# Kernel optimization log

Measured on AMD Instinct MI355X. Metric: run time of the kernel, lower is better.

The kernel has to match this reference:

```python
import jax, jax.numpy as jnp
import numpy as np

N, T, F = 64, 2048, 256
PAD_VALUE = 0.0  # mode='constant'


def setup_inputs() -> dict:
    key = jax.random.key(0)
    kx, ks, kl = jax.random.split(key, 3)
    x = jax.random.normal(kx, (N, T, F), dtype=jnp.float32)
    slices = jnp.sort(jax.random.randint(ks, (N, 2), 0, T, dtype=jnp.int64), axis=-1)
    lens = jax.random.randint(kl, (N,), 0, T, dtype=jnp.int64)
    return {"x": x, "slices": slices, "lens": lens}


def reference(x, slices, lens):
    # x: (N, T, F); slices: (N, 2) [start, end); lens: (N,)
    n, t_dim, f_dim = x.shape
    start = slices[:, 0]
    end = slices[:, 1]
    chunk_lens = jnp.clip(end - start, 0)
    empty = chunk_lens == 0
    left_pad = jnp.where(empty, 0, jnp.clip(-start, 0))  # 0 here since start>=0
    start_ = jnp.clip(start, 0)
    end_ = jnp.minimum(end, lens)
    slice_lens = jnp.clip(end_ - start_, 0)
    # Static Tp = T (valid since generated chunks satisfy Tp <= T).
    t = jnp.arange(t_dim)  # (Tp,)
    # source index in x for each output position (shifted by left_pad)
    src = start_[:, None] + t[None, :] - left_pad[:, None]  # (N, Tp)
    valid = (t[None, :] >= left_pad[:, None]) & (
        t[None, :] < (left_pad + slice_lens)[:, None]
    )  # (N, Tp)
    src_c = jnp.clip(src, 0, t_dim - 1)
    gathered = jnp.take_along_axis(x, src_c[:, :, None], axis=1)  # (N, Tp, F)
    chunks = jnp.where(valid[:, :, None], gathered, jnp.float32(PAD_VALUE))
    return chunks, chunk_lens
```

## Files before the change

### kernel.cpp

```cpp
#include <hip/hip_runtime.h>

constexpr int N  = 64;
constexpr int T  = 2048;
constexpr int F  = 256;
constexpr int F4   = F / 4;
constexpr int ROW4 = T * F4;
constexpr int TOTAL4 = N * ROW4;

__global__ void __launch_bounds__(256)
chunk_by_slices_kernel(const float4* __restrict__ x4,
                       const int*    __restrict__ slices,
                       const int*    __restrict__ lens,
                       float4*       __restrict__ out4,
                       float*        __restrict__ out_lens)
{
    const int tid0   = blockIdx.x * blockDim.x + threadIdx.x;
    const int stride = gridDim.x * blockDim.x;

    if (tid0 < N) {
        const int s = slices[2 * tid0];
        const int e = slices[2 * tid0 + 1];
        int cl = e - s;
        if (cl < 0) cl = 0;
        out_lens[tid0] = (float)cl;
    }

    for (int i = tid0; i < TOTAL4; i += stride) {
        const int n  = i >> 17;
        const int t  = (i >> 6) & (T - 1);
        const int f4 = i & (F4 - 1);

        const int s = slices[2 * n];
        const int e = slices[2 * n + 1];
        const int L = lens[n];

        const int  cl    = e - s;
        const bool empty = (cl <= 0);
        int lp = -s; if (lp < 0) lp = 0; if (empty) lp = 0;
        int s_ = s;  if (s_ < 0) s_ = 0;
        int e_ = (e < L) ? e : L;
        int sl = e_ - s_; if (sl < 0) sl = 0;

        const bool valid = (t >= lp) && (t < lp + sl);

        float4 v = make_float4(0.f, 0.f, 0.f, 0.f);
        if (valid) {
            int src = s_ + t - lp;
            src = (src < 0) ? 0 : ((src > T - 1) ? T - 1 : src);
            v = x4[n * ROW4 + src * F4 + f4];
        }
        out4[i] = v;
    }
}

extern "C" void kernel_launch(void* const* d_in, const int* in_sizes, int n_in,
                              void* d_out, int out_size, void* d_ws, size_t ws_size,
                              hipStream_t stream) {
    const float4* x4     = (const float4*)d_in[0];
    const int*    slices = (const int*)d_in[1];
    const int*    lens   = (const int*)d_in[2];

    float* out      = (float*)d_out;
    float4* out4    = (float4*)out;
    float* out_lens = out + (size_t)N * T * F;

    const int threads = 256;
    const int blocks  = 2048;
    chunk_by_slices_kernel<<<blocks, threads, 0, stream>>>(x4, slices, lens, out4, out_lens);
}
```

Before: 220.3 us.

## Assign each block a fixed row chunk and use nontemporal loads/stores

Replaces the grid-stride loop with a fixed mapping: each block handles 64 time rows of one batch element. The per-row slice bounds are then computed once per block instead of once per element. Loads and stores switch to nontemporal builtins on native vector types so streaming data bypasses cache retention. Each thread does a fixed 16 iterations, unrolled by four.

```diff
diff --git a/kernel.cpp b/kernel.cpp
--- a/kernel.cpp
+++ b/kernel.cpp
@@ -5,66 +5,69 @@
 constexpr int F  = 256;
 constexpr int F4   = F / 4;
 constexpr int ROW4 = T * F4;
-constexpr int TOTAL4 = N * ROW4;
+
+typedef float floatx4 __attribute__((ext_vector_type(4)));
 
 __global__ void __launch_bounds__(256)
-chunk_by_slices_kernel(const float4* __restrict__ x4,
-                       const int*    __restrict__ slices,
-                       const int*    __restrict__ lens,
-                       float4*       __restrict__ out4,
-                       float*        __restrict__ out_lens)
+chunk_by_slices_kernel(const floatx4* __restrict__ x4,
+                       const int*     __restrict__ slices,
+                       const int*     __restrict__ lens,
+                       floatx4*       __restrict__ out4,
+                       float*         __restrict__ out_lens)
 {
-    const int tid0   = blockIdx.x * blockDim.x + threadIdx.x;
-    const int stride = gridDim.x * blockDim.x;
+    const int n      = blockIdx.x >> 5;
+    const int tchunk = blockIdx.x & 31;
+    const int t0     = tchunk << 6;
 
-    if (tid0 < N) {
-        const int s = slices[2 * tid0];
-        const int e = slices[2 * tid0 + 1];
-        int cl = e - s;
-        if (cl < 0) cl = 0;
-        out_lens[tid0] = (float)cl;
+    const int s = slices[2 * n];
+    const int e = slices[2 * n + 1];
+    const int L = lens[n];
+
+    const int  cl    = e - s;
+    const bool empty = (cl <= 0);
+    int lp = -s; if (lp < 0) lp = 0; if (empty) lp = 0;
+    int s_ = s;  if (s_ < 0) s_ = 0;
+    int e_ = (e < L) ? e : L;
+    int sl = e_ - s_; if (sl < 0) sl = 0;
+    const int vlo = lp;
+    const int vhi = lp + sl;
+
+    if (tchunk == 0 && threadIdx.x == 0) {
+        out_lens[n] = (float)(cl < 0 ? 0 : cl);
     }
 
-    for (int i = tid0; i < TOTAL4; i += stride) {
-        const int n  = i >> 17;
-        const int t  = (i >> 6) & (T - 1);
-        const int f4 = i & (F4 - 1);
+    const int f4   = threadIdx.x & 63;
+    const int wrow = threadIdx.x >> 6;
 
-        const int s = slices[2 * n];
-        const int e = slices[2 * n + 1];
-        const int L = lens[n];
+    const floatx4 zero = (floatx4)0.0f;
+    const floatx4* __restrict__ xrow = x4 + (size_t)n * ROW4;
+    floatx4* __restrict__ orow       = out4 + (size_t)n * ROW4;
 
-        const int  cl    = e - s;
-        const bool empty = (cl <= 0);
-        int lp = -s; if (lp < 0) lp = 0; if (empty) lp = 0;
-        int s_ = s;  if (s_ < 0) s_ = 0;
-        int e_ = (e < L) ? e : L;
-        int sl = e_ - s_; if (sl < 0) sl = 0;
-
-        const bool valid = (t >= lp) && (t < lp + sl);
-
-        float4 v = make_float4(0.f, 0.f, 0.f, 0.f);
-        if (valid) {
+    #pragma unroll 4
+    for (int r = 0; r < 16; ++r) {
+        const int t = t0 + (r << 2) + wrow;
+        floatx4 v = zero;
+        if (t >= vlo && t < vhi) {
             int src = s_ + t - lp;
             src = (src < 0) ? 0 : ((src > T - 1) ? T - 1 : src);
-            v = x4[n * ROW4 + src * F4 + f4];
+            v = __builtin_nontemporal_load(&xrow[src * F4 + f4]);
         }
-        out4[i] = v;
+        __builtin_nontemporal_store(v, &orow[t * F4 + f4]);
     }
 }
 
 extern "C" void kernel_launch(void* const* d_in, const int* in_sizes, int n_in,
                               void* d_out, int out_size, void* d_ws, size_t ws_size,
                               hipStream_t stream) {
-    const float4* x4     = (const float4*)d_in[0];
+    const floatx4* x4    = (const floatx4*)d_in[0];
     const int*    slices = (const int*)d_in[1];
     const int*    lens   = (const int*)d_in[2];
 
     float* out      = (float*)d_out;
-    float4* out4    = (float4*)out;
+    floatx4* out4   = (floatx4*)out;
     float* out_lens = out + (size_t)N * T * F;
 
     const int threads = 256;
-    const int blocks  = 2048;
+    const int blocks  = N * 32;
     chunk_by_slices_kernel<<<blocks, threads, 0, stream>>>(x4, slices, lens, out4, out_lens);
 }
```

Measured after the change: 219.7 us. Within noise of the previous version (-0.3%).
